# Optimization experiments

Hardware: AMD Instinct MI355X
Metric: run time of the kernel (lower is better)

The kernel has to match this reference:

```python
import jax, jax.numpy as jnp
import numpy as np

NUM_NODES = 100000
EMB_DIM = 64
OUT_C = 64
K = 3
NUM_EDGES = 1600000


def setup_inputs() -> dict:
    key = jax.random.key(0)
    k1, k2, k3, k4 = jax.random.split(key, 4)
    x_indices = jnp.arange(NUM_NODES, dtype=jnp.int64)
    ei = jax.random.randint(k1, (2, NUM_EDGES), 0, NUM_NODES, dtype=jnp.int64)
    # learned params: embedding table + final linear of SGConv
    emb_weight = jax.random.normal(k2, (NUM_NODES, EMB_DIM), dtype=jnp.float32)
    lin_w = jax.random.normal(k3, (OUT_C, EMB_DIM), dtype=jnp.float32) / np.sqrt(EMB_DIM)
    lin_b = jax.random.normal(k4, (OUT_C,), dtype=jnp.float32) * 0.01
    return {"x_indices": x_indices, "ei": ei, "emb_weight": emb_weight,
            "lin_w": lin_w, "lin_b": lin_b}


def _sgconv(x, ei, lin_w, lin_b, k_hops):
    """PyG SGConv: (D^-1/2 (A+I) D^-1/2)^K X, then Linear."""
    n = x.shape[0]
    row, col = ei[0], ei[1]
    loops = jnp.arange(n, dtype=ei.dtype)
    row = jnp.concatenate([row, loops])
    col = jnp.concatenate([col, loops])
    ones = jnp.ones(row.shape[0], dtype=x.dtype)
    deg = jax.ops.segment_sum(ones, col, num_segments=n)  # in-degree incl. self-loops
    dinv = jnp.where(deg > 0, jax.lax.rsqrt(deg), 0.0)
    norm = dinv[row] * dinv[col]  # [E+N]
    for _ in range(k_hops):
        # gather source features, scale, scatter-add to targets
        x = jax.ops.segment_sum(x[row] * norm[:, None], col, num_segments=n)
    return x @ lin_w.T + lin_b


def reference(x_indices, ei, emb_weight, lin_w, lin_b):
    x = emb_weight[x_indices]  # [N, EMB_DIM] embedding lookup
    return _sgconv(x, ei, lin_w, lin_b, K)
```

## Files before the change

kernel.cpp:

```cpp
#include <hip/hip_runtime.h>
#include <hip/hip_bf16.h>
#include <math.h>


#define FLAG_MX 0
#define FLAG_ME 1
#define SH 9
#define WC 512
#define CH 4096
#define RMASK 0x7FFFFFu

using short8 = __attribute__((ext_vector_type(8))) short;
using f32x4 = __attribute__((ext_vector_type(4))) float;

__device__ inline int idx_at(const void* p, long long i, int mode) {
    switch (mode) {
        case 1: return (int)((const long long*)p)[i];
        case 2: return (int)((const float*)p)[i];
        case 3: return (int)((const double*)p)[i];
        default: return ((const int*)p)[i];
    }
}

__device__ inline unsigned short f2bf(float f) {
    union { float f; unsigned u; } v; v.f = f;
    unsigned r = v.u + 0x7FFFu + ((v.u >> 16) & 1u);
    return (unsigned short)(r >> 16);
}
__device__ inline float bflo(unsigned d) { union { unsigned u; float f; } v; v.u = d << 16; return v.f; }
__device__ inline float bfhi(unsigned d) { union { unsigned u; float f; } v; v.u = d & 0xFFFF0000u; return v.f; }
__device__ inline unsigned pk(float a, float b) {
    return (unsigned)f2bf(a) | ((unsigned)f2bf(b) << 16);
}

__device__ int detect_me_block(const void* ei, int n, int* sbuf) {
    int t = threadIdx.x;
    int oke = 15;
    const int* w = (const int*)ei;
    const long long* L = (const long long*)ei;
    const float* f = (const float*)ei;
    const double* d = (const double*)ei;
    for (int k = t; k < 2048; k += 256) {
        if (!((unsigned)w[k] < (unsigned)n)) oke &= ~1;
        long long lv = L[k];
        if (!(lv >= 0 && lv < (long long)n)) oke &= ~2;
        float fv = f[k];
        if (!(fv >= 0.f && fv < (float)n && fv == truncf(fv))) oke &= ~4;
        double dv = d[k];
        if (!(dv >= 0.0 && dv < (double)n && dv == trunc(dv))) oke &= ~8;
    }
    sbuf[t] = oke;
    __syncthreads();
    for (int st = 128; st; st >>= 1) {
        if (t < st) sbuf[t] &= sbuf[t + st];
        __syncthreads();
    }
    int r = sbuf[0];
    __syncthreads();
    return (r & 2) ? 1 : (r & 8) ? 3 : (r & 4) ? 2 : 0;
}

__device__ int detect_mx_block(const void* xidx, int* sbuf) {
    int t = threadIdx.x;
    int okx = 15;
    const int* w = (const int*)xidx;
    const long long* L = (const long long*)xidx;
    const float* f = (const float*)xidx;
    const double* d = (const double*)xidx;
    for (int k = t; k < 2048; k += 256) {
        if (w[k] != k) okx &= ~1;
        if (L[k] != (long long)k) okx &= ~2;
        if (!(f[k] == (float)k)) okx &= ~4;
        if (!(d[k] == (double)k)) okx &= ~8;
    }
    sbuf[t] = okx;
    __syncthreads();
    for (int st = 128; st; st >>= 1) {
        if (t < st) sbuf[t] &= sbuf[t + st];
        __syncthreads();
    }
    int r = sbuf[0];
    __syncthreads();
    return (r & 2) ? 1 : (r & 8) ? 3 : (r & 4) ? 2 : 0;
}

__global__ void __launch_bounds__(256) k_p1(
        const void* __restrict__ ei, const void* __restrict__ xidx,
        long long E, int n, int NBUK, int NBLK,
        int* __restrict__ bhist, int* __restrict__ flags) {
    __shared__ int hist[256];
    __shared__ int sbuf[256];
    int t = threadIdx.x;
    int blk = blockIdx.x;
    int me = detect_me_block(ei, n, sbuf);
    if (blk == 0) {
        int mx = detect_mx_block(xidx, sbuf);
        if (t == 0) { flags[FLAG_ME] = me; flags[FLAG_MX] = mx; }
    }
    long long base = (long long)blk * CH;
    int cnt = (int)min((long long)CH, E - base);
    hist[t] = 0;
    __syncthreads();
    for (int i = t; i < cnt; i += 256) {
        int c = idx_at(ei, E + base + i, me);
        int b = min(c >> SH, NBUK - 1);
        atomicAdd(&hist[b], 1);
    }
    __syncthreads();
    if (t < NBUK) bhist[(size_t)t * NBLK + blk] = hist[t];
}

__global__ void __launch_bounds__(256) k_p2a(
        int* __restrict__ bhist, int* __restrict__ gcount, int NBLK) {
    __shared__ int s[256];
    int b = blockIdx.x;
    int t = threadIdx.x;
    int* row = bhist + (size_t)b * NBLK;
    int carry = 0;
    for (int base = 0; base < NBLK; base += 256) {
        int i = base + t;
        int v = (i < NBLK) ? row[i] : 0;
        s[t] = v;
        __syncthreads();
        for (int st = 1; st < 256; st <<= 1) {
            int add = (t >= st) ? s[t - st] : 0;
            __syncthreads();
            s[t] += add;
            __syncthreads();
        }
        if (i < NBLK) row[i] = carry + s[t] - v;
        int total = s[255];
        __syncthreads();
        carry += total;
    }
    if (t == 0) gcount[b] = carry;
}

__device__ void scan_gcount(const int* gcount, int NBUK, int* p, int* gb_ex) {
    int t = threadIdx.x;
    int v = (t < NBUK) ? gcount[t] : 0;
    p[t] = v;
    __syncthreads();
    for (int st = 1; st < 256; st <<= 1) {
        int add = (t >= st) ? p[t - st] : 0;
        __syncthreads();
        p[t] += add;
        __syncthreads();
    }
    gb_ex[t] = p[t] - v;
    __syncthreads();
}

__device__ void scan_gcount_512(const int* gcount, int NBUK, int* p, int* gb_ex) {
    int t = threadIdx.x;
    int v = (t < 256) ? ((t < NBUK) ? gcount[t] : 0) : 0;
    if (t < 256) p[t] = v;
    __syncthreads();
    for (int st = 1; st < 256; st <<= 1) {
        int add = (t >= st && t < 256) ? p[t - st] : 0;
        __syncthreads();
        if (t < 256) p[t] += add;
        __syncthreads();
    }
    if (t < 256) gb_ex[t] = p[t] - v;
    __syncthreads();
}

__global__ void __launch_bounds__(256) k_p3(
        const void* __restrict__ ei, long long E, int n, int NBUK, int NBLK,
        const int* __restrict__ bhist, const int* __restrict__ gcount,
        unsigned* __restrict__ gstag, const int* __restrict__ flags) {
    __shared__ int hist[256], lbase[256], rsv[256], lcur[256], s[256], gb[256];
    __shared__ unsigned stage[CH];
    int t = threadIdx.x;
    int blk = blockIdx.x;
    scan_gcount(gcount, NBUK, s, gb);
    long long base = (long long)blk * CH;
    int cnt = (int)min((long long)CH, E - base);
    int me = flags[FLAG_ME];
    hist[t] = 0;
    __syncthreads();
    for (int i = t; i < cnt; i += 256) {
        int c = idx_at(ei, E + base + i, me);
        atomicAdd(&hist[min(c >> SH, NBUK - 1)], 1);
    }
    __syncthreads();
    int v = hist[t];
    s[t] = v;
    __syncthreads();
    for (int st = 1; st < 256; st <<= 1) {
        int add = (t >= st) ? s[t - st] : 0;
        __syncthreads();
        s[t] += add;
        __syncthreads();
    }
    lbase[t] = s[t] - v;
    lcur[t] = s[t] - v;
    if (t < NBUK) rsv[t] = gb[t] + bhist[(size_t)t * NBLK + blk];
    __syncthreads();
    for (int i = t; i < cnt; i += 256) {
        long long e = base + i;
        int r = idx_at(ei, e, me);
        int c = idx_at(ei, E + e, me);
        int b = min(c >> SH, NBUK - 1);
        unsigned pkv = ((unsigned)r & RMASK) |
                       (((unsigned)(c - (b << SH)) & (WC - 1)) << 23);
        int slot = atomicAdd(&lcur[b], 1);
        stage[slot] = pkv;
    }
    __syncthreads();
    for (int i = t; i < cnt; i += 256) {
        unsigned pkv = stage[i];
        int lo = 0, hi = NBUK - 1;
        while (lo < hi) {
            int mid = (lo + hi + 1) >> 1;
            if (lbase[mid] <= i) lo = mid; else hi = mid - 1;
        }
        gstag[rsv[lo] + (i - lbase[lo])] = pkv;
    }
}

__global__ void __launch_bounds__(512) k_p4(
        const unsigned* __restrict__ gstag, const int* __restrict__ gcount,
        int* __restrict__ off, float* __restrict__ dinv,
        int* __restrict__ rowidx, int n, int NBUK) {
    __shared__ int hist[WC], lofs[WC], cur[WC], p[512], gb[256];
    int t = threadIdx.x;
    int b = blockIdx.x;
    int cbase = b << SH;
    scan_gcount_512(gcount, NBUK, p, gb);
    int e0 = gb[b];
    int e1 = e0 + gcount[b];
    int cnt = e1 - e0;
    if (b == NBUK - 1 && t == 0) off[n] = e1;
    hist[t] = 0;
    __syncthreads();
    for (int i = t; i < cnt; i += 512) {
        atomicAdd(&hist[gstag[e0 + i] >> 23], 1);
    }
    __syncthreads();
    int v = hist[t];
    p[t] = v;
    __syncthreads();
    for (int st = 1; st < 512; st <<= 1) {
        int add = (t >= st) ? p[t - st] : 0;
        __syncthreads();
        p[t] += add;
        __syncthreads();
    }
    int excl = p[t] - v;
    lofs[t] = excl;
    cur[t] = excl;
    __syncthreads();
    int ncols = n - cbase;
    if (ncols < 0) ncols = 0;
    if (ncols > WC) ncols = WC;
    if (t < ncols) {
        off[cbase + t] = e0 + lofs[t];
        dinv[cbase + t] = rsqrtf((float)(hist[t] + 1));
    }
    for (int i = t; i < cnt; i += 512) {
        unsigned pkv = gstag[e0 + i];
        int cl = (int)(pkv >> 23);
        int slot = atomicAdd(&cur[cl], 1);
        rowidx[e0 + slot] = (int)(pkv & RMASK);
    }
}

__global__ void __launch_bounds__(256) k_z0(
        const void* __restrict__ xidx, const float4* __restrict__ emb4,
        const float* __restrict__ dinv, uint4* __restrict__ z, int n,
        const int* __restrict__ flags) {
    int i = blockIdx.x * 256 + threadIdx.x;
    if (i >= n * 8) return;
    int node = i >> 3, q = i & 7;
    int xi = idx_at(xidx, node, flags[FLAG_MX]);
    if ((unsigned)xi >= (unsigned)n) xi = 0;
    float d = dinv[node];
    float4 a = emb4[(long long)xi * 16 + q * 2];
    float4 b = emb4[(long long)xi * 16 + q * 2 + 1];
    uint4 o;
    o.x = pk(a.x * d, a.y * d);
    o.y = pk(a.z * d, a.w * d);
    o.z = pk(b.x * d, b.y * d);
    o.w = pk(b.z * d, b.w * d);
    z[(long long)node * 8 + q] = o;
}

__device__ inline void acc8(float* acc, uint4 s) {
    acc[0] += bflo(s.x); acc[1] += bfhi(s.x);
    acc[2] += bflo(s.y); acc[3] += bfhi(s.y);
    acc[4] += bflo(s.z); acc[5] += bfhi(s.z);
    acc[6] += bflo(s.w); acc[7] += bfhi(s.w);
}

__global__ void __launch_bounds__(256) k_hop(
        const uint4* __restrict__ zin, uint4* __restrict__ zout,
        const float* __restrict__ dinv, const int* __restrict__ off,
        const int* __restrict__ rowidx, int n, int last) {
    int tid = blockIdx.x * 256 + threadIdx.x;
    int node = tid >> 3;
    int q = tid & 7;
    if (node >= n) return;
    float acc[8];
    {
        uint4 s = zin[(long long)node * 8 + q];
        acc[0] = bflo(s.x); acc[1] = bfhi(s.x);
        acc[2] = bflo(s.y); acc[3] = bfhi(s.y);
        acc[4] = bflo(s.z); acc[5] = bfhi(s.z);
        acc[6] = bflo(s.w); acc[7] = bfhi(s.w);
    }
    int e0 = off[node], e1 = off[node + 1];
    int e = e0;
    for (; e + 4 <= e1; e += 4) {
        int r0 = rowidx[e + 0];
        int r1 = rowidx[e + 1];
        int r2 = rowidx[e + 2];
        int r3 = rowidx[e + 3];
        uint4 s0 = zin[(long long)r0 * 8 + q];
        uint4 s1 = zin[(long long)r1 * 8 + q];
        uint4 s2 = zin[(long long)r2 * 8 + q];
        uint4 s3 = zin[(long long)r3 * 8 + q];
        acc8(acc, s0);
        acc8(acc, s1);
        acc8(acc, s2);
        acc8(acc, s3);
    }
    for (; e < e1; e++) {
        int r = rowidx[e];
        acc8(acc, zin[(long long)r * 8 + q]);
    }
    float d = dinv[node];
    float sc = last ? d : d * d;
    uint4 o;
    o.x = pk(acc[0] * sc, acc[1] * sc);
    o.y = pk(acc[2] * sc, acc[3] * sc);
    o.z = pk(acc[4] * sc, acc[5] * sc);
    o.w = pk(acc[6] * sc, acc[7] * sc);
    zout[(long long)node * 8 + q] = o;
}

__global__ void __launch_bounds__(256) k_lin_mfma(
        const short8* __restrict__ x8, const float* __restrict__ w,
        const float* __restrict__ b, float* __restrict__ out, int n, int ntiles) {
    int lane = threadIdx.x & 63;
    int wv = threadIdx.x >> 6;
    int col = lane & 15, quad = lane >> 4;

    short8 bw[4][2];
#pragma unroll
    for (int tN = 0; tN < 4; tN++)
#pragma unroll
        for (int s = 0; s < 2; s++) {
            const float* src = w + (tN * 16 + col) * 64 + s * 32 + quad * 8;
            short8 v;
#pragma unroll
            for (int j = 0; j < 8; j++) v[j] = (short)f2bf(src[j]);
            bw[tN][s] = v;
        }
    float bv[4];
#pragma unroll
    for (int tN = 0; tN < 4; tN++) bv[tN] = b[tN * 16 + col];

    int tile = blockIdx.x * 4 + wv;
    if (tile >= ntiles) return;
    int node0 = tile * 16;

    short8 a[2];
    int m = node0 + col;
#pragma unroll
    for (int s = 0; s < 2; s++) {
        if (m < n) a[s] = x8[(size_t)m * 8 + s * 4 + quad];
        else a[s] = short8{0, 0, 0, 0, 0, 0, 0, 0};
    }
#pragma unroll
    for (int tN = 0; tN < 4; tN++) {
        f32x4 acc = {bv[tN], bv[tN], bv[tN], bv[tN]};
        acc = __builtin_amdgcn_mfma_f32_16x16x32_bf16(a[0], bw[tN][0], acc, 0, 0, 0);
        acc = __builtin_amdgcn_mfma_f32_16x16x32_bf16(a[1], bw[tN][1], acc, 0, 0, 0);
#pragma unroll
        for (int r = 0; r < 4; r++) {
            int node = node0 + quad * 4 + r;
            if (node < n) out[(size_t)node * 64 + tN * 16 + col] = acc[r];
        }
    }
}

extern "C" void kernel_launch(void* const* d_in, const int* in_sizes, int n_in,
                              void* d_out, int out_size, void* d_ws, size_t ws_size,
                              hipStream_t stream) {
    const void* xidx = d_in[0];
    const void* ei = d_in[1];
    const float* emb = (const float*)d_in[2];
    const float* w = (const float*)d_in[3];
    const float* b = (const float*)d_in[4];

    const int n = in_sizes[0];
    const long long E = in_sizes[1] / 2;
    int NBUK = (int)((n + WC - 1) >> SH);
    if (NBUK > 256) NBUK = 256;
    const int NBLK = (int)((E + CH - 1) / CH);

    char* p = (char*)d_ws;
    auto alloc = [&](size_t bytes) -> void* {
        void* r = (void*)p;
        p += (bytes + 255) & ~(size_t)255;
        return r;
    };
    int* flags = (int*)alloc(256);
    float* dinv = (float*)alloc((size_t)n * 4);
    int* off = (int*)alloc((size_t)(n + 1) * 4);
    int* gcount = (int*)alloc(257 * 4);
    int* bhist = (int*)alloc((size_t)NBLK * NBUK * 4);
    int* rowidx = (int*)alloc((size_t)E * 4);
    uint4* zA = (uint4*)alloc((size_t)n * 64 * 2);
    uint4* zS = (uint4*)d_out;

    unsigned* gstag;
    if ((size_t)E * 4 <= (size_t)n * 64 * 2)
        gstag = (unsigned*)((char*)d_out + (size_t)n * 64 * 2);
    else
        gstag = (unsigned*)alloc((size_t)E * 4);

    k_p1<<<NBLK, 256, 0, stream>>>(ei, xidx, E, n, NBUK, NBLK, bhist, flags);
    k_p2a<<<NBUK, 256, 0, stream>>>(bhist, gcount, NBLK);
    k_p3<<<NBLK, 256, 0, stream>>>(ei, E, n, NBUK, NBLK, bhist, gcount, gstag, flags);
    k_p4<<<NBUK, 512, 0, stream>>>(gstag, gcount, off, dinv, rowidx, n, NBUK);

    const int gF = (n * 8 + 255) / 256;
    const int ntiles = (n + 15) / 16;
    const int gM = (ntiles + 3) / 4;

    k_z0<<<gF, 256, 0, stream>>>(xidx, (const float4*)emb, dinv, zS, n, flags);
    k_hop<<<gF, 256, 0, stream>>>(zS, zA, dinv, off, rowidx, n, 0);
    k_hop<<<gF, 256, 0, stream>>>(zA, zS, dinv, off, rowidx, n, 0);
    k_hop<<<gF, 256, 0, stream>>>(zS, zA, dinv, off, rowidx, n, 1);
    k_lin_mfma<<<gM, 256, 0, stream>>>((const short8*)zA, w, b, (float*)d_out,
                                       n, ntiles);
}
```

Measured before the change: 259.2 us.

## Fuse final propagation hop into MFMA linear kernel and sort per-node neighbor lists

The last aggregation hop is merged into the bf16 MFMA linear kernel. Each node's neighbor sum is built in registers, scaled by dinv, packed to bf16 and fed straight into the MFMA, so the last intermediate feature buffer is never written or read back and one launch is dropped. The CSR build kernel also insertion-sorts each column's source indices in shared memory (degree up to 48), aiming for more ordered gathers. The trade-offs are fewer threads per node in the fused hop, a large shared-memory allocation in k_p4 that may lower its occupancy, and serial per-thread sorting work.

```diff
diff --git a/kernel.cpp b/kernel.cpp
--- a/kernel.cpp
+++ b/kernel.cpp
@@ -9,6 +9,7 @@
 #define WC 512
 #define CH 4096
 #define RMASK 0x7FFFFFu
+#define DCAP 48
 
 using short8 = __attribute__((ext_vector_type(8))) short;
 using f32x4 = __attribute__((ext_vector_type(4))) float;
@@ -225,6 +226,7 @@
         int* __restrict__ off, float* __restrict__ dinv,
         int* __restrict__ rowidx, int n, int NBUK) {
     __shared__ int hist[WC], lofs[WC], cur[WC], p[512], gb[256];
+    __shared__ int sortbuf[512 * (DCAP + 1)];
     int t = threadIdx.x;
     int b = blockIdx.x;
     int cbase = b << SH;
@@ -264,6 +266,23 @@
         int cl = (int)(pkv >> 23);
         int slot = atomicAdd(&cur[cl], 1);
         rowidx[e0 + slot] = (int)(pkv & RMASK);
+    }
+    __threadfence_block();
+    __syncthreads();
+    if (t < ncols) {
+        int deg = hist[t];
+        if (deg > 1 && deg <= DCAP) {
+            int base = e0 + lofs[t];
+            int* loc = sortbuf + t * (DCAP + 1);
+            for (int i = 0; i < deg; i++) loc[i] = rowidx[base + i];
+            for (int i = 1; i < deg; i++) {
+                int key = loc[i];
+                int j = i - 1;
+                while (j >= 0 && loc[j] > key) { loc[j + 1] = loc[j]; j--; }
+                loc[j + 1] = key;
+            }
+            for (int i = 0; i < deg; i++) rowidx[base + i] = loc[i];
+        }
     }
 }
 
@@ -340,9 +359,11 @@
     zout[(long long)node * 8 + q] = o;
 }
 
-__global__ void __launch_bounds__(256) k_lin_mfma(
-        const short8* __restrict__ x8, const float* __restrict__ w,
-        const float* __restrict__ b, float* __restrict__ out, int n, int ntiles) {
+__global__ void __launch_bounds__(256) k_hop_lin(
+        const uint4* __restrict__ zin, const float* __restrict__ dinv,
+        const int* __restrict__ off, const int* __restrict__ rowidx,
+        const float* __restrict__ w, const float* __restrict__ bias,
+        float* __restrict__ out, int n, int ntiles) {
     int lane = threadIdx.x & 63;
     int wv = threadIdx.x >> 6;
     int col = lane & 15, quad = lane >> 4;
@@ -353,35 +374,72 @@
 #pragma unroll
         for (int s = 0; s < 2; s++) {
             const float* src = w + (tN * 16 + col) * 64 + s * 32 + quad * 8;
-            short8 v;
-#pragma unroll
-            for (int j = 0; j < 8; j++) v[j] = (short)f2bf(src[j]);
-            bw[tN][s] = v;
+            short8 vv;
+#pragma unroll
+            for (int j = 0; j < 8; j++) vv[j] = (short)f2bf(src[j]);
+            bw[tN][s] = vv;
         }
     float bv[4];
 #pragma unroll
-    for (int tN = 0; tN < 4; tN++) bv[tN] = b[tN * 16 + col];
+    for (int tN = 0; tN < 4; tN++) bv[tN] = bias[tN * 16 + col];
 
     int tile = blockIdx.x * 4 + wv;
     if (tile >= ntiles) return;
-    int node0 = tile * 16;
-
-    short8 a[2];
-    int m = node0 + col;
-#pragma unroll
-    for (int s = 0; s < 2; s++) {
-        if (m < n) a[s] = x8[(size_t)m * 8 + s * 4 + quad];
-        else a[s] = short8{0, 0, 0, 0, 0, 0, 0, 0};
+    int node = tile * 16 + col;
+
+    float acc[16];
+#pragma unroll
+    for (int j = 0; j < 16; j++) acc[j] = 0.f;
+    float sc = 0.f;
+    if (node < n) {
+        uint4 sa = zin[(long long)node * 8 + quad];
+        uint4 sb = zin[(long long)node * 8 + quad + 4];
+        acc8(acc, sa);
+        acc8(acc + 8, sb);
+        int e0 = off[node], e1 = off[node + 1];
+        int e = e0;
+        for (; e + 4 <= e1; e += 4) {
+            int r0 = rowidx[e + 0];
+            int r1 = rowidx[e + 1];
+            int r2 = rowidx[e + 2];
+            int r3 = rowidx[e + 3];
+            uint4 a0 = zin[(long long)r0 * 8 + quad];
+            uint4 b0 = zin[(long long)r0 * 8 + quad + 4];
+            uint4 a1 = zin[(long long)r1 * 8 + quad];
+            uint4 b1 = zin[(long long)r1 * 8 + quad + 4];
+            uint4 a2 = zin[(long long)r2 * 8 + quad];
+            uint4 b2 = zin[(long long)r2 * 8 + quad + 4];
+            uint4 a3 = zin[(long long)r3 * 8 + quad];
+            uint4 b3 = zin[(long long)r3 * 8 + quad + 4];
+            acc8(acc, a0); acc8(acc + 8, b0);
+            acc8(acc, a1); acc8(acc + 8, b1);
+            acc8(acc, a2); acc8(acc + 8, b2);
+            acc8(acc, a3); acc8(acc + 8, b3);
+        }
+        for (; e < e1; e++) {
+            int r = rowidx[e];
+            uint4 sa2 = zin[(long long)r * 8 + quad];
+            uint4 sb2 = zin[(long long)r * 8 + quad + 4];
+            acc8(acc, sa2);
+            acc8(acc + 8, sb2);
+        }
+        sc = dinv[node];
+    }
+    short8 a0f, a1f;
+#pragma unroll
+    for (int j = 0; j < 8; j++) {
+        a0f[j] = (short)f2bf(acc[j] * sc);
+        a1f[j] = (short)f2bf(acc[8 + j] * sc);
     }
 #pragma unroll
     for (int tN = 0; tN < 4; tN++) {
-        f32x4 acc = {bv[tN], bv[tN], bv[tN], bv[tN]};
-        acc = __builtin_amdgcn_mfma_f32_16x16x32_bf16(a[0], bw[tN][0], acc, 0, 0, 0);
-        acc = __builtin_amdgcn_mfma_f32_16x16x32_bf16(a[1], bw[tN][1], acc, 0, 0, 0);
+        f32x4 c = {bv[tN], bv[tN], bv[tN], bv[tN]};
+        c = __builtin_amdgcn_mfma_f32_16x16x32_bf16(a0f, bw[tN][0], c, 0, 0, 0);
+        c = __builtin_amdgcn_mfma_f32_16x16x32_bf16(a1f, bw[tN][1], c, 0, 0, 0);
 #pragma unroll
         for (int r = 0; r < 4; r++) {
-            int node = node0 + quad * 4 + r;
-            if (node < n) out[(size_t)node * 64 + tN * 16 + col] = acc[r];
+            int nd = tile * 16 + quad * 4 + r;
+            if (nd < n) out[(size_t)nd * 64 + tN * 16 + col] = c[r];
         }
     }
 }
@@ -431,10 +489,9 @@
     const int ntiles = (n + 15) / 16;
     const int gM = (ntiles + 3) / 4;
 
-    k_z0<<<gF, 256, 0, stream>>>(xidx, (const float4*)emb, dinv, zS, n, flags);
+    k_z0<<<gF, 256, 0, stream>>>(xidx, (const float4*)emb, dinv, zA, n, flags);
+    k_hop<<<gF, 256, 0, stream>>>(zA, zS, dinv, off, rowidx, n, 0);
     k_hop<<<gF, 256, 0, stream>>>(zS, zA, dinv, off, rowidx, n, 0);
-    k_hop<<<gF, 256, 0, stream>>>(zA, zS, dinv, off, rowidx, n, 0);
-    k_hop<<<gF, 256, 0, stream>>>(zS, zA, dinv, off, rowidx, n, 1);
-    k_lin_mfma<<<gM, 256, 0, stream>>>((const short8*)zA, w, b, (float*)d_out,
-                                       n, ntiles);
-}
+    k_hop_lin<<<gM, 256, 0, stream>>>(zA, dinv, off, rowidx, w, b,
+                                      (float*)d_out, n, ntiles);
+}
```

Result: slower. 311.0 us (+20.0%).
